# Optimization experiments

Measured on AMD Instinct MI355X. Metric: run time of the kernel, lower is better.

Reference implementation:

```python
import jax, jax.numpy as jnp
import numpy as np

B, T, ROLL, RHY, COND, Z1, H = 4096, 32, 130, 3, 12, 128, 1024
IN1 = Z1 + ROLL + RHY + COND  # 273, grucell_1 input size


def _gru_cell(x, h, w_ih, w_hh, b_ih, b_hh):
    # PyTorch GRUCell math. w_ih: [3H, in], w_hh: [3H, H]
    gi = x @ w_ih.T + b_ih
    gh = h @ w_hh.T + b_hh
    i_r, i_z, i_n = jnp.split(gi, 3, axis=1)
    h_r, h_z, h_n = jnp.split(gh, 3, axis=1)
    r = jax.nn.sigmoid(i_r + h_r)
    z = jax.nn.sigmoid(i_z + h_z)
    n = jnp.tanh(i_n + r * h_n)
    return (1.0 - z) * n + z * h


def setup_inputs() -> dict:
    key = jax.random.key(0)
    ks = jax.random.split(key, 20)
    s = 0.02
    inp = {
        "z1": jax.random.normal(ks[0], (B, Z1), jnp.float32),
        "dis1_mean": jax.random.normal(ks[1], (B, Z1), jnp.float32),
        "dis1_std": jax.random.uniform(ks[2], (B, Z1), jnp.float32),
        "dis2_mean": jax.random.normal(ks[3], (B, Z1), jnp.float32),
        "dis2_std": jax.random.uniform(ks[4], (B, Z1), jnp.float32),
        "recon_rhythm": jax.random.normal(ks[5], (B, T, RHY), jnp.float32),
        "sample": jax.random.normal(ks[6], (B, T, ROLL), jnp.float32),
        "condition": jax.random.normal(ks[7], (B, T, COND), jnp.float32),
        "iteration": 1000,
        # grucell_1
        "w_ih1": jax.random.normal(ks[8], (3 * H, IN1), jnp.float32) * s,
        "w_hh1": jax.random.normal(ks[9], (3 * H, H), jnp.float32) * s,
        "b_ih1": jax.random.normal(ks[10], (3 * H,), jnp.float32) * s,
        "b_hh1": jax.random.normal(ks[11], (3 * H,), jnp.float32) * s,
        # grucell_2
        "w_ih2": jax.random.normal(ks[12], (3 * H, H), jnp.float32) * s,
        "w_hh2": jax.random.normal(ks[13], (3 * H, H), jnp.float32) * s,
        "b_ih2": jax.random.normal(ks[14], (3 * H,), jnp.float32) * s,
        "b_hh2": jax.random.normal(ks[15], (3 * H,), jnp.float32) * s,
        # linear_init_1: z1 -> H
        "w_init": jax.random.normal(ks[16], (H, Z1), jnp.float32) * s,
        "b_init": jax.random.normal(ks[17], (H,), jnp.float32) * s,
        # linear_out_1: H -> roll
        "w_out": jax.random.normal(ks[18], (ROLL, H), jnp.float32) * s,
        "b_out": jax.random.normal(ks[19], (ROLL,), jnp.float32) * s,
    }
    return inp


def reference(z1, dis1_mean, dis1_std, dis2_mean, dis2_std, recon_rhythm, sample,
              condition, iteration, w_ih1, w_hh1, b_ih1, b_hh1, w_ih2, w_hh2,
              b_ih2, b_hh2, w_init, b_init, w_out, b_out):
    # Eval-mode final_decoder: teacher forcing off, argmax one-hot sampling.
    h1_0 = jnp.tanh(z1 @ w_init.T + b_init)
    out0 = jnp.zeros((B, ROLL), z1.dtype).at[:, -1].set(1.0)
    h2_0 = jnp.zeros((B, H), z1.dtype)  # overwritten at step 0

    rhy_t = jnp.transpose(recon_rhythm, (1, 0, 2))   # [T,B,RHY]
    cond_t = jnp.transpose(condition, (1, 0, 2))     # [T,B,COND]

    def step(carry, xs):
        out, h1, h2 = carry
        i, r_i, c_i = xs
        inp = jnp.concatenate([out, r_i, z1, c_i], axis=1)  # [B, IN1]
        h1 = _gru_cell(inp, h1, w_ih1, w_hh1, b_ih1, b_hh1)
        h2 = jnp.where(i == 0, h1, h2)  # hx[1] = hx[0] on first step
        h2 = _gru_cell(h1, h2, w_ih2, w_hh2, b_ih2, b_hh2)
        logp = jax.nn.log_softmax(h2 @ w_out.T + b_out, axis=1)  # [B,ROLL]
        out = jax.nn.one_hot(jnp.argmax(logp, axis=1), ROLL, dtype=logp.dtype)
        return (out, h1, h2), logp

    xs = (jnp.arange(T), rhy_t, cond_t)
    _, logps = jax.lax.scan(step, (out0, h1_0, h2_0), xs)
    recon = jnp.transpose(logps, (1, 0, 2))  # [B,T,ROLL]
    return (recon, recon_rhythm, dis1_mean, dis1_std, dis2_mean, dis2_std)
```

## Files before the change

### kernel.cpp

```cpp
#include <hip/hip_runtime.h>
#include <stdint.h>

typedef unsigned short u16;
typedef unsigned int u32;
typedef __attribute__((ext_vector_type(4))) float f32x4;
typedef __attribute__((ext_vector_type(8))) short short8;

#define MFMA16(a, b, c) __builtin_amdgcn_mfma_f32_16x16x32_bf16(a, b, c, 0, 0, 0)

#define B_SZ   4096
#define H_SZ   1024
#define T_SZ   32
#define NROLL  130
#define EXTK   192
#define NCPAD  144

__device__ __forceinline__ u16 f2b(float f) {
  u32 u = __float_as_uint(f);
  u += 0x7FFFu + ((u >> 16) & 1u);
  return (u16)(u >> 16);
}
__device__ __forceinline__ float sigm(float x) { return 1.f / (1.f + __expf(-x)); }

__device__ __forceinline__ void gld16(const void* g, const void* lds) {
  __builtin_amdgcn_global_load_lds(
      (const __attribute__((address_space(1))) u32*)(uintptr_t)g,
      (__attribute__((address_space(3))) u32*)(u32)(uintptr_t)lds, 16, 0, 0);
}

__global__ void cvt_kernel(const float* __restrict__ s, u16* __restrict__ d, int n) {
  int i = blockIdx.x * 256 + threadIdx.x;
  if (i < n) d[i] = f2b(s[i]);
}

__global__ void build_wout_kernel(const float* __restrict__ w, u16* __restrict__ d) {
  int i = blockIdx.x * 256 + threadIdx.x;
  int r = i >> 10, c = i & 1023;
  d[i] = f2b(r < NROLL ? w[r * H_SZ + c] : 0.f);
}

__global__ void build_wext_kernel(const float* __restrict__ w, u16* __restrict__ d) {
  int i = blockIdx.x * 256 + threadIdx.x;
  int j = i / EXTK, k = i % EXTK;
  float v = 0.f;
  if (k < 3)        v = w[j * 273 + 130 + k];
  else if (k < 15)  v = w[j * 273 + 261 + (k - 3)];
  else if (k < 143) v = w[j * 273 + 133 + (k - 15)];
  d[i] = f2b(v);
}

__global__ void build_wih1T_kernel(const float* __restrict__ w, float* __restrict__ d) {
  int i = blockIdx.x * 256 + threadIdx.x;
  if (i >= NROLL * 3072) return;
  int c = i / 3072, j = i % 3072;
  d[i] = w[j * 273 + c];
}

__global__ void build_aext_kernel(const float* __restrict__ rhy, const float* __restrict__ cond,
                                  const float* __restrict__ z1, u16* __restrict__ d) {
  long long i = (long long)blockIdx.x * 256 + threadIdx.x;
  int t = (int)(i / (B_SZ * EXTK));
  int r = (int)(i % (B_SZ * EXTK));
  int b = r / EXTK, k = r % EXTK;
  float v = 0.f;
  if (k < 3)        v = rhy[b * (T_SZ * 3) + t * 3 + k];
  else if (k < 15)  v = cond[b * (T_SZ * 12) + t * 12 + (k - 3)];
  else if (k < 143) v = z1[b * 128 + (k - 15)];
  d[i] = f2b(v);
}

__global__ void init_amax_kernel(int* __restrict__ a) {
  a[blockIdx.x * 256 + threadIdx.x] = NROLL - 1;
}

__global__ __launch_bounds__(256, 2)
void init_h1_mfma_kernel(const u16* __restrict__ Az,
                         const u16* __restrict__ Wz,
                         const float* __restrict__ b_init,
                         float* __restrict__ h1f, u16* __restrict__ h1b) {
  __shared__ u16 As[128 * 64];
  __shared__ u16 Ws[64 * 64];
  const int tid = threadIdx.x;
  const int lane = tid & 63, wv = tid >> 6;
  const int wm = wv >> 1, wn = wv & 1;
  const int lr = lane & 15, lk = lane >> 4;
  const int Mbase = blockIdx.x * 128, Nbase = blockIdx.y * 64;

  f32x4 zero = {0.f, 0.f, 0.f, 0.f};
  f32x4 acc[4][2];
#pragma unroll
  for (int m = 0; m < 4; ++m)
#pragma unroll
    for (int n = 0; n < 2; ++n) acc[m][n] = zero;

  for (int it = 0; it < 2; ++it) {
#pragma unroll
    for (int i = 0; i < 4; ++i) {
      int seg = i * 256 + tid, row = seg >> 3, c8 = seg & 7;
      gld16(Az + (size_t)(Mbase + row) * 128 + it * 64 + c8 * 8, As + ((i * 256 + (wv << 6)) << 3));
    }
#pragma unroll
    for (int i = 0; i < 2; ++i) {
      int seg = i * 256 + tid, row = seg >> 3, c8 = seg & 7;
      gld16(Wz + (size_t)(Nbase + row) * 128 + it * 64 + c8 * 8, Ws + ((i * 256 + (wv << 6)) << 3));
    }
    __syncthreads();
#pragma unroll
    for (int kk = 0; kk < 2; ++kk) {
      short8 af[4];
#pragma unroll
      for (int m = 0; m < 4; ++m)
        af[m] = *(const short8*)(As + (((wm << 6) + (m << 4) + lr) << 6) + kk * 32 + (lk << 3));
      short8 bw[2];
#pragma unroll
      for (int n = 0; n < 2; ++n)
        bw[n] = *(const short8*)(Ws + ((((wn << 5) + (n << 4) + lr)) << 6) + kk * 32 + (lk << 3));
#pragma unroll
      for (int m = 0; m < 4; ++m)
#pragma unroll
        for (int n = 0; n < 2; ++n)
          acc[m][n] = MFMA16(af[m], bw[n], acc[m][n]);
    }
    __syncthreads();
  }

  int hcol[2];
  hcol[0] = Nbase + (wn << 5) + lr;
  hcol[1] = hcol[0] + 16;
#pragma unroll
  for (int m = 0; m < 4; ++m) {
#pragma unroll
    for (int q = 0; q < 4; ++q) {
      int b = Mbase + (wm << 6) + (m << 4) + (lk << 2) + q;
      size_t ho = (size_t)b << 10;
#pragma unroll
      for (int n = 0; n < 2; ++n) {
        int h = hcol[n];
        float v = tanhf(acc[m][n][q] + b_init[h]);
        h1f[ho + h] = v;
        h1b[ho + h] = f2b(v);
      }
    }
  }
}

__global__ __launch_bounds__(256, 2)
void gru1_kernel(const u16* __restrict__ Ah,
                 const u16* __restrict__ Whh,
                 const u16* __restrict__ Ae,
                 const u16* __restrict__ Wex,
                 const float* __restrict__ gT,
                 const float* __restrict__ bih, const float* __restrict__ bhh,
                 const int* __restrict__ amax,
                 float* __restrict__ h1f, u16* __restrict__ h1o) {
  __shared__ u16 smem[40960];
  u16* As = smem;
  u16* Wsm = smem + 16384;
  const int tid = threadIdx.x;
  const int lane = tid & 63, wv = tid >> 6;
  const int wm = wv >> 1, wn = wv & 1;
  const int lr = lane & 15, lk = lane >> 4;
  const int Mbase = blockIdx.x * 128, Nbase = blockIdx.y * 64;

  f32x4 zero = {0.f, 0.f, 0.f, 0.f};
  f32x4 acc_r[4][2], acc_z[4][2], acc_hn[4][2], acc_in[4][2];
#pragma unroll
  for (int m = 0; m < 4; ++m)
#pragma unroll
    for (int n = 0; n < 2; ++n) { acc_r[m][n] = zero; acc_z[m][n] = zero; acc_hn[m][n] = zero; acc_in[m][n] = zero; }

#pragma unroll 1
  for (int it = 0; it < 8; ++it) {
#pragma unroll
    for (int i = 0; i < 8; ++i) {
      int seg = i * 256 + tid, row = seg >> 4, c16 = (seg & 15) ^ (row & 7);
      gld16(Ah + (size_t)(Mbase + row) * 1024 + it * 128 + c16 * 8, As + ((i * 256 + (wv << 6)) << 3));
    }
#pragma unroll
    for (int i = 0; i < 12; ++i) {
      int seg = i * 256 + tid, gr = seg >> 4, c16 = (seg & 15) ^ (gr & 7);
      int gg = gr >> 6, r = gr & 63;
      gld16(Whh + ((size_t)(gg << 10) + Nbase + r) * 1024 + it * 128 + c16 * 8,
            Wsm + ((i * 256 + (wv << 6)) << 3));
    }
    __syncthreads();
    __builtin_amdgcn_s_setprio(1);
#pragma unroll
    for (int kk = 0; kk < 4; ++kk) {
      int gc = (kk << 2) + lk;
      short8 af[4];
#pragma unroll
      for (int m = 0; m < 4; ++m) {
        int row = (wm << 6) + (m << 4) + lr;
        af[m] = *(const short8*)(As + (row << 7) + ((gc ^ (row & 7)) << 3));
      }
      short8 bw[3][2];
#pragma unroll
      for (int g = 0; g < 3; ++g)
#pragma unroll
        for (int n = 0; n < 2; ++n) {
          int row = (g << 6) + (wn << 5) + (n << 4) + lr;
          bw[g][n] = *(const short8*)(Wsm + (row << 7) + ((gc ^ (row & 7)) << 3));
        }
#pragma unroll
      for (int m = 0; m < 4; ++m)
#pragma unroll
        for (int n = 0; n < 2; ++n) {
          acc_r[m][n] = MFMA16(af[m], bw[0][n], acc_r[m][n]);
          acc_z[m][n] = MFMA16(af[m], bw[1][n], acc_z[m][n]);
          acc_hn[m][n] = MFMA16(af[m], bw[2][n], acc_hn[m][n]);
        }
    }
    __builtin_amdgcn_s_setprio(0);
    __syncthreads();
  }

#pragma unroll 1
  for (int e = 0; e < 3; ++e) {
#pragma unroll
    for (int i = 0; i < 4; ++i) {
      int seg = i * 256 + tid, row = seg >> 3, c8 = (seg & 7) ^ (row & 7);
      gld16(Ae + (size_t)(Mbase + row) * EXTK + e * 64 + c8 * 8, As + ((i * 256 + (wv << 6)) << 3));
    }
#pragma unroll
    for (int i = 0; i < 6; ++i) {
      int seg = i * 256 + tid, gr = seg >> 3, c8 = (seg & 7) ^ (gr & 7);
      int gg = gr >> 6, r = gr & 63;
      gld16(Wex + ((size_t)(gg << 10) + Nbase + r) * EXTK + e * 64 + c8 * 8,
            Wsm + ((i * 256 + (wv << 6)) << 3));
    }
    __syncthreads();
    __builtin_amdgcn_s_setprio(1);
#pragma unroll
    for (int kk = 0; kk < 2; ++kk) {
      int gc = (kk << 2) + lk;
      short8 af[4];
#pragma unroll
      for (int m = 0; m < 4; ++m) {
        int row = (wm << 6) + (m << 4) + lr;
        af[m] = *(const short8*)(As + (row << 6) + ((gc ^ (row & 7)) << 3));
      }
      short8 bw[3][2];
#pragma unroll
      for (int g = 0; g < 3; ++g)
#pragma unroll
        for (int n = 0; n < 2; ++n) {
          int row = (g << 6) + (wn << 5) + (n << 4) + lr;
          bw[g][n] = *(const short8*)(Wsm + (row << 6) + ((gc ^ (row & 7)) << 3));
        }
#pragma unroll
      for (int m = 0; m < 4; ++m)
#pragma unroll
        for (int n = 0; n < 2; ++n) {
          acc_r[m][n] = MFMA16(af[m], bw[0][n], acc_r[m][n]);
          acc_z[m][n] = MFMA16(af[m], bw[1][n], acc_z[m][n]);
          acc_in[m][n] = MFMA16(af[m], bw[2][n], acc_in[m][n]);
        }
    }
    __builtin_amdgcn_s_setprio(0);
    __syncthreads();
  }

  int hcol[2];
  hcol[0] = Nbase + (wn << 5) + lr;
  hcol[1] = hcol[0] + 16;
  float bi0[2], bi1[2], bi2[2], bh0[2], bh1[2], bh2[2];
#pragma unroll
  for (int n = 0; n < 2; ++n) {
    int h = hcol[n];
    bi0[n] = bih[h]; bi1[n] = bih[1024 + h]; bi2[n] = bih[2048 + h];
    bh0[n] = bhh[h]; bh1[n] = bhh[1024 + h]; bh2[n] = bhh[2048 + h];
  }
#pragma unroll
  for (int m = 0; m < 4; ++m) {
#pragma unroll
    for (int q = 0; q < 4; ++q) {
      int b = Mbase + (wm << 6) + (m << 4) + (lk << 2) + q;
      const float* gRow = gT + (size_t)amax[b] * 3072;
      size_t ho = (size_t)b << 10;
#pragma unroll
      for (int n = 0; n < 2; ++n) {
        int h = hcol[n];
        float rp = acc_r[m][n][q] + bi0[n] + bh0[n] + gRow[h];
        float zp = acc_z[m][n][q] + bi1[n] + bh1[n] + gRow[1024 + h];
        float inp = acc_in[m][n][q] + bi2[n] + gRow[2048 + h];
        float hnp = acc_hn[m][n][q] + bh2[n];
        float r = sigm(rp), z = sigm(zp);
        float nn = tanhf(inp + r * hnp);
        float hv = (1.f - z) * nn + z * h1f[ho + h];
        h1f[ho + h] = hv;
        h1o[ho + h] = f2b(hv);
      }
    }
  }
}

__global__ __launch_bounds__(256, 2)
void gru2_kernel(const u16* __restrict__ A1,
                 const u16* __restrict__ A2,
                 const u16* __restrict__ Wi,
                 const u16* __restrict__ Wh,
                 const float* __restrict__ bih, const float* __restrict__ bhh,
                 const float* __restrict__ hpf,
                 float* __restrict__ h2f, u16* __restrict__ h2o) {
  __shared__ u16 As1[128 * 64];
  __shared__ u16 As2[128 * 64];
  __shared__ u16 Ws[384 * 64];
  const int tid = threadIdx.x;
  const int lane = tid & 63, wv = tid >> 6;
  const int wm = wv >> 1, wn = wv & 1;
  const int lr = lane & 15, lk = lane >> 4;
  const int Mbase = blockIdx.x * 128, Nbase = blockIdx.y * 64;

  f32x4 zero = {0.f, 0.f, 0.f, 0.f};
  f32x4 acc_r[4][2], acc_z[4][2], acc_hn[4][2], acc_in[4][2];
#pragma unroll
  for (int m = 0; m < 4; ++m)
#pragma unroll
    for (int n = 0; n < 2; ++n) { acc_r[m][n] = zero; acc_z[m][n] = zero; acc_hn[m][n] = zero; acc_in[m][n] = zero; }

#pragma unroll 1
  for (int it = 0; it < 16; ++it) {
#pragma unroll
    for (int i = 0; i < 4; ++i) {
      int seg = i * 256 + tid, row = seg >> 3, c8 = (seg & 7) ^ (row & 7);
      size_t go = (size_t)(Mbase + row) * 1024 + it * 64 + c8 * 8;
      gld16(A1 + go, As1 + ((i * 256 + (wv << 6)) << 3));
      gld16(A2 + go, As2 + ((i * 256 + (wv << 6)) << 3));
    }
#pragma unroll
    for (int i = 0; i < 12; ++i) {
      int seg = i * 256 + tid, gr = seg >> 3, c8 = (seg & 7) ^ (gr & 7);
      int s = gr >> 6, r = gr & 63;
      const u16* Wm = (s < 3) ? Wi : Wh;
      int gate = (s < 3) ? s : (s - 3);
      gld16(Wm + ((size_t)(gate << 10) + Nbase + r) * 1024 + it * 64 + c8 * 8,
            Ws + ((i * 256 + (wv << 6)) << 3));
    }
    __syncthreads();
    __builtin_amdgcn_s_setprio(1);
#pragma unroll
    for (int kk = 0; kk < 2; ++kk) {
      int gc = (kk << 2) + lk;
      short8 a1[4], a2[4];
#pragma unroll
      for (int m = 0; m < 4; ++m) {
        int row = (wm << 6) + (m << 4) + lr;
        int off = (row << 6) + ((gc ^ (row & 7)) << 3);
        a1[m] = *(const short8*)(As1 + off);
        a2[m] = *(const short8*)(As2 + off);
      }
      short8 bw[6][2];
#pragma unroll
      for (int s = 0; s < 6; ++s)
#pragma unroll
        for (int n = 0; n < 2; ++n) {
          int row = (s << 6) + (wn << 5) + (n << 4) + lr;
          bw[s][n] = *(const short8*)(Ws + (row << 6) + ((gc ^ (row & 7)) << 3));
        }
#pragma unroll
      for (int m = 0; m < 4; ++m)
#pragma unroll
        for (int n = 0; n < 2; ++n) {
          acc_r[m][n] = MFMA16(a1[m], bw[0][n], acc_r[m][n]);
          acc_r[m][n] = MFMA16(a2[m], bw[3][n], acc_r[m][n]);
          acc_z[m][n] = MFMA16(a1[m], bw[1][n], acc_z[m][n]);
          acc_z[m][n] = MFMA16(a2[m], bw[4][n], acc_z[m][n]);
          acc_in[m][n] = MFMA16(a1[m], bw[2][n], acc_in[m][n]);
          acc_hn[m][n] = MFMA16(a2[m], bw[5][n], acc_hn[m][n]);
        }
    }
    __builtin_amdgcn_s_setprio(0);
    __syncthreads();
  }

  int hcol[2];
  hcol[0] = Nbase + (wn << 5) + lr;
  hcol[1] = hcol[0] + 16;
  float bi0[2], bi1[2], bi2[2], bh0[2], bh1[2], bh2[2];
#pragma unroll
  for (int n = 0; n < 2; ++n) {
    int h = hcol[n];
    bi0[n] = bih[h]; bi1[n] = bih[1024 + h]; bi2[n] = bih[2048 + h];
    bh0[n] = bhh[h]; bh1[n] = bhh[1024 + h]; bh2[n] = bhh[2048 + h];
  }
#pragma unroll
  for (int m = 0; m < 4; ++m) {
#pragma unroll
    for (int q = 0; q < 4; ++q) {
      int b = Mbase + (wm << 6) + (m << 4) + (lk << 2) + q;
      size_t ho = (size_t)b << 10;
#pragma unroll
      for (int n = 0; n < 2; ++n) {
        int h = hcol[n];
        float r = sigm(acc_r[m][n][q] + bi0[n] + bh0[n]);
        float z = sigm(acc_z[m][n][q] + bi1[n] + bh1[n]);
        float nn = tanhf(acc_in[m][n][q] + bi2[n] + r * (acc_hn[m][n][q] + bh2[n]));
        float hv = (1.f - z) * nn + z * hpf[ho + h];
        h2f[ho + h] = hv;
        h2o[ho + h] = f2b(hv);
      }
    }
  }
}

__global__ __launch_bounds__(128)
void out_kernel(const u16* __restrict__ A,
                const u16* __restrict__ W,
                const float* __restrict__ b_out,
                float* __restrict__ recon, int* __restrict__ amax_out, int t) {
  __shared__ u16 As[16 * 64];
  __shared__ u16 Ws[144 * 64];
  __shared__ float redm[2][16], reds[2][16], logZs[16];
  __shared__ int redi[2][16];
  const int tid = threadIdx.x;
  const int lane = tid & 63, wv = tid >> 6;
  const int lr = lane & 15, lk = lane >> 4;
  const int bb = blockIdx.x;
  const int nf0 = wv ? 5 : 0;
  const int nfn = wv ? 4 : 5;

  f32x4 zero = {0.f, 0.f, 0.f, 0.f};
  f32x4 acc[5];
#pragma unroll
  for (int j = 0; j < 5; ++j) acc[j] = zero;

  float bo[5];
#pragma unroll
  for (int j = 0; j < 5; ++j) {
    int col = ((nf0 + j) << 4) + lr;
    bo[j] = (j < nfn && col < NROLL) ? b_out[col] : -1e30f;
  }

#pragma unroll 1
  for (int it = 0; it < 16; ++it) {
    {
      int seg = tid, row = seg >> 3, c8 = seg & 7;
      gld16(A + (size_t)(bb * 16 + row) * 1024 + it * 64 + c8 * 8, As + ((wv << 6) << 3));
    }
#pragma unroll
    for (int i = 0; i < 9; ++i) {
      int seg = i * 128 + tid, row = seg >> 3, c8 = seg & 7;
      gld16(W + (size_t)row * 1024 + it * 64 + c8 * 8, Ws + ((i * 128 + (wv << 6)) << 3));
    }
    __syncthreads();
#pragma unroll
    for (int kk = 0; kk < 2; ++kk) {
      short8 af = *(const short8*)(As + (lr << 6) + kk * 32 + (lk << 3));
#pragma unroll 5
      for (int j = 0; j < 5; ++j) {
        if (j < nfn) {
          short8 bw = *(const short8*)(Ws + ((((nf0 + j) << 4) + lr) << 6) + kk * 32 + (lk << 3));
          acc[j] = MFMA16(af, bw, acc[j]);
        }
      }
    }
    __syncthreads();
  }

#pragma unroll
  for (int q = 0; q < 4; ++q) {
    int r = (lk << 2) + q;
    float vmax = -1e30f; int vidx = 0;
#pragma unroll 5
    for (int j = 0; j < 5; ++j) {
      if (j < nfn) {
        int col = ((nf0 + j) << 4) + lr;
        float x = acc[j][q] + bo[j];
        if (x > vmax) { vmax = x; vidx = col; }
      }
    }
    for (int d = 1; d < 16; d <<= 1) {
      float om = __shfl_xor(vmax, d);
      int oi = __shfl_xor(vidx, d);
      if (om > vmax || (om == vmax && oi < vidx)) { vmax = om; vidx = oi; }
    }
    float s = 0.f;
#pragma unroll 5
    for (int j = 0; j < 5; ++j) {
      if (j < nfn) s += __expf(acc[j][q] + bo[j] - vmax);
    }
    for (int d = 1; d < 16; d <<= 1) s += __shfl_xor(s, d);
    if (lr == 0) { redm[wv][r] = vmax; reds[wv][r] = s; redi[wv][r] = vidx; }
  }
  __syncthreads();

  if (tid < 16) {
    float m0 = redm[0][tid], m1 = redm[1][tid];
    float s0 = reds[0][tid], s1 = reds[1][tid];
    float M = fmaxf(m0, m1);
    float S = s0 * __expf(m0 - M) + s1 * __expf(m1 - M);
    logZs[tid] = M + __logf(S);
    amax_out[bb * 16 + tid] = (m1 > m0) ? redi[1][tid] : redi[0][tid];
  }
  __syncthreads();

#pragma unroll
  for (int q = 0; q < 4; ++q) {
    int r = (lk << 2) + q;
    int b = bb * 16 + r;
    float lz = logZs[r];
#pragma unroll 5
    for (int j = 0; j < 5; ++j) {
      if (j < nfn) {
        int col = ((nf0 + j) << 4) + lr;
        if (col < NROLL)
          recon[(size_t)b * (T_SZ * NROLL) + t * NROLL + col] = acc[j][q] + bo[j] - lz;
      }
    }
  }
}

extern "C" void kernel_launch(void* const* d_in, const int* in_sizes, int n_in,
                              void* d_out, int out_size, void* d_ws, size_t ws_size,
                              hipStream_t stream) {
  const float* z1    = (const float*)d_in[0];
  const float* d1m   = (const float*)d_in[1];
  const float* d1s   = (const float*)d_in[2];
  const float* d2m   = (const float*)d_in[3];
  const float* d2s   = (const float*)d_in[4];
  const float* rhy   = (const float*)d_in[5];
  const float* cond  = (const float*)d_in[7];
  const float* w_ih1 = (const float*)d_in[9];
  const float* w_hh1 = (const float*)d_in[10];
  const float* b_ih1 = (const float*)d_in[11];
  const float* b_hh1 = (const float*)d_in[12];
  const float* w_ih2 = (const float*)d_in[13];
  const float* w_hh2 = (const float*)d_in[14];
  const float* b_ih2 = (const float*)d_in[15];
  const float* b_hh2 = (const float*)d_in[16];
  const float* w_init = (const float*)d_in[17];
  const float* b_init = (const float*)d_in[18];
  const float* w_out  = (const float*)d_in[19];
  const float* b_out  = (const float*)d_in[20];
  float* out = (float*)d_out;

  char* ws = (char*)d_ws;
  size_t off = 0;
  auto alloc = [&](size_t bytes) -> void* {
    off = (off + 255) & ~(size_t)255;
    void* p = ws + off;
    off += bytes;
    return p;
  };
  u16* whh1_b = (u16*)alloc((size_t)3072 * 1024 * 2);
  u16* wih2_b = (u16*)alloc((size_t)3072 * 1024 * 2);
  u16* whh2_b = (u16*)alloc((size_t)3072 * 1024 * 2);
  u16* wout_b = (u16*)alloc((size_t)NCPAD * 1024 * 2);
  u16* wext_b = (u16*)alloc((size_t)3072 * EXTK * 2);
  float* wih1T = (float*)alloc((size_t)NROLL * 3072 * 4);
  u16* aext   = (u16*)alloc((size_t)T_SZ * B_SZ * EXTK * 2);
  float* h1f  = (float*)alloc((size_t)B_SZ * H_SZ * 4);
  float* h2f  = (float*)alloc((size_t)B_SZ * H_SZ * 4);
  u16* h1b[2];
  h1b[0] = (u16*)alloc((size_t)B_SZ * H_SZ * 2);
  h1b[1] = (u16*)alloc((size_t)B_SZ * H_SZ * 2);
  u16* h2b[2];
  h2b[0] = (u16*)alloc((size_t)B_SZ * H_SZ * 2);
  h2b[1] = (u16*)alloc((size_t)B_SZ * H_SZ * 2);
  int* amax = (int*)alloc((size_t)B_SZ * 4);
  u16* z1b    = (u16*)alloc((size_t)B_SZ * 128 * 2);
  u16* winitb = (u16*)alloc((size_t)H_SZ * 128 * 2);

  const int NW = 3072 * 1024;
  cvt_kernel<<<(NW + 255) / 256, 256, 0, stream>>>(w_hh1, whh1_b, NW);
  cvt_kernel<<<(NW + 255) / 256, 256, 0, stream>>>(w_ih2, wih2_b, NW);
  cvt_kernel<<<(NW + 255) / 256, 256, 0, stream>>>(w_hh2, whh2_b, NW);
  cvt_kernel<<<(B_SZ * 128 + 255) / 256, 256, 0, stream>>>(z1, z1b, B_SZ * 128);
  cvt_kernel<<<(H_SZ * 128 + 255) / 256, 256, 0, stream>>>(w_init, winitb, H_SZ * 128);
  build_wout_kernel<<<(NCPAD * 1024) / 256, 256, 0, stream>>>(w_out, wout_b);
  build_wext_kernel<<<(3072 * EXTK) / 256, 256, 0, stream>>>(w_ih1, wext_b);
  build_wih1T_kernel<<<(NROLL * 3072 + 255) / 256, 256, 0, stream>>>(w_ih1, wih1T);
  build_aext_kernel<<<(T_SZ * B_SZ * EXTK) / 256, 256, 0, stream>>>(rhy, cond, z1, aext);
  init_h1_mfma_kernel<<<dim3(B_SZ / 128, H_SZ / 64), 256, 0, stream>>>(z1b, winitb, b_init, h1f, h1b[0]);
  init_amax_kernel<<<B_SZ / 256, 256, 0, stream>>>(amax);

  size_t o_rhy = (size_t)B_SZ * T_SZ * NROLL;
  size_t o_d1m = o_rhy + (size_t)B_SZ * T_SZ * 3;
  size_t o_d1s = o_d1m + (size_t)B_SZ * 128;
  size_t o_d2m = o_d1s + (size_t)B_SZ * 128;
  size_t o_d2s = o_d2m + (size_t)B_SZ * 128;
  hipMemcpyAsync(out + o_rhy, rhy, (size_t)B_SZ * T_SZ * 3 * 4, hipMemcpyDeviceToDevice, stream);
  hipMemcpyAsync(out + o_d1m, d1m, (size_t)B_SZ * 128 * 4, hipMemcpyDeviceToDevice, stream);
  hipMemcpyAsync(out + o_d1s, d1s, (size_t)B_SZ * 128 * 4, hipMemcpyDeviceToDevice, stream);
  hipMemcpyAsync(out + o_d2m, d2m, (size_t)B_SZ * 128 * 4, hipMemcpyDeviceToDevice, stream);
  hipMemcpyAsync(out + o_d2s, d2s, (size_t)B_SZ * 128 * 4, hipMemcpyDeviceToDevice, stream);

  dim3 ggrid(B_SZ / 128, H_SZ / 64);
  for (int t = 0; t < T_SZ; ++t) {
    const u16* h1in = h1b[t & 1];
    u16* h1out = h1b[(t & 1) ^ 1];
    gru1_kernel<<<ggrid, 256, 0, stream>>>(h1in, whh1_b, aext + (size_t)t * B_SZ * EXTK,
                                           wext_b, wih1T, b_ih1, b_hh1, amax, h1f, h1out);
    const u16* h2in = (t == 0) ? (const u16*)h1out : h2b[t & 1];
    const float* hpf = (t == 0) ? h1f : h2f;
    u16* h2out = h2b[(t & 1) ^ 1];
    gru2_kernel<<<ggrid, 256, 0, stream>>>(h1out, h2in, wih2_b, whh2_b, b_ih2, b_hh2,
                                           hpf, h2f, h2out);
    out_kernel<<<B_SZ / 16, 128, 0, stream>>>(h2out, wout_b, b_out, out, amax, t);
  }
  (void)in_sizes; (void)n_in; (void)out_size; (void)ws_size;
}
```

Baseline: 3.663 ms.

## Prepack GRU2 weights in MFMA fragment order and load them directly from global

Adds a one-time prepass that packs w_ih2 and w_hh2 as bf16 in per-lane MFMA operand order. gru2_kernel then reads its B fragments straight from global memory with one coalesced 16-byte load per lane, and the LDS weight tile and its staging loads are removed. This cuts LDS traffic and shared-memory footprint, which may raise occupancy. The cost is weight loads issued inside the compute loop, no longer overlapped through LDS, and the two waves sharing an N-slice now fetch the same weights separately, relying on L2 to absorb it.

Result: slower. 4.462 ms (+21.8%).

```diff
diff --git a/kernel.cpp b/kernel.cpp
--- a/kernel.cpp
+++ b/kernel.cpp
@@ -67,6 +67,21 @@
   else if (k < 15)  v = cond[b * (T_SZ * 12) + t * 12 + (k - 3)];
   else if (k < 143) v = z1[b * 128 + (k - 15)];
   d[i] = f2b(v);
+}
+
+__global__ void build_wpk2_kernel(const float* __restrict__ wi, const float* __restrict__ wh,
+                                  u16* __restrict__ d) {
+  int i = blockIdx.x * 256 + threadIdx.x;
+  int j = i & 7;
+  int lane = (i >> 3) & 63;
+  int kb = (i >> 9) & 31;
+  int nb = (i >> 14) & 63;
+  int g = i >> 20;
+  int n = nb * 16 + (lane & 15);
+  int k = kb * 32 + (lane >> 4) * 8 + j;
+  const float* src = (g < 3) ? wi : wh;
+  int gg = (g < 3) ? g : g - 3;
+  d[i] = f2b(src[(size_t)(gg * 1024 + n) * 1024 + k]);
 }
 
 __global__ void init_amax_kernel(int* __restrict__ a) {
@@ -298,19 +313,18 @@
 __global__ __launch_bounds__(256, 2)
 void gru2_kernel(const u16* __restrict__ A1,
                  const u16* __restrict__ A2,
-                 const u16* __restrict__ Wi,
-                 const u16* __restrict__ Wh,
+                 const u16* __restrict__ Wpk,
                  const float* __restrict__ bih, const float* __restrict__ bhh,
                  const float* __restrict__ hpf,
                  float* __restrict__ h2f, u16* __restrict__ h2o) {
   __shared__ u16 As1[128 * 64];
   __shared__ u16 As2[128 * 64];
-  __shared__ u16 Ws[384 * 64];
   const int tid = threadIdx.x;
   const int lane = tid & 63, wv = tid >> 6;
   const int wm = wv >> 1, wn = wv & 1;
   const int lr = lane & 15, lk = lane >> 4;
   const int Mbase = blockIdx.x * 128, Nbase = blockIdx.y * 64;
+  const int nbB = (Nbase >> 4) + (wn << 1);
 
   f32x4 zero = {0.f, 0.f, 0.f, 0.f};
   f32x4 acc_r[4][2], acc_z[4][2], acc_hn[4][2], acc_in[4][2];
@@ -328,19 +342,17 @@
       gld16(A1 + go, As1 + ((i * 256 + (wv << 6)) << 3));
       gld16(A2 + go, As2 + ((i * 256 + (wv << 6)) << 3));
     }
-#pragma unroll
-    for (int i = 0; i < 12; ++i) {
-      int seg = i * 256 + tid, gr = seg >> 3, c8 = (seg & 7) ^ (gr & 7);
-      int s = gr >> 6, r = gr & 63;
-      const u16* Wm = (s < 3) ? Wi : Wh;
-      int gate = (s < 3) ? s : (s - 3);
-      gld16(Wm + ((size_t)(gate << 10) + Nbase + r) * 1024 + it * 64 + c8 * 8,
-            Ws + ((i * 256 + (wv << 6)) << 3));
-    }
     __syncthreads();
     __builtin_amdgcn_s_setprio(1);
 #pragma unroll
     for (int kk = 0; kk < 2; ++kk) {
+      int kb = (it << 1) + kk;
+      short8 bw[6][2];
+#pragma unroll
+      for (int g = 0; g < 6; ++g)
+#pragma unroll
+        for (int nf = 0; nf < 2; ++nf)
+          bw[g][nf] = *(const short8*)(Wpk + ((((size_t)((g << 6) + nbB + nf) << 5) + kb) << 9) + (lane << 3));
       int gc = (kk << 2) + lk;
       short8 a1[4], a2[4];
 #pragma unroll
@@ -350,14 +362,6 @@
         a1[m] = *(const short8*)(As1 + off);
         a2[m] = *(const short8*)(As2 + off);
       }
-      short8 bw[6][2];
-#pragma unroll
-      for (int s = 0; s < 6; ++s)
-#pragma unroll
-        for (int n = 0; n < 2; ++n) {
-          int row = (s << 6) + (wn << 5) + (n << 4) + lr;
-          bw[s][n] = *(const short8*)(Ws + (row << 6) + ((gc ^ (row & 7)) << 3));
-        }
 #pragma unroll
       for (int m = 0; m < 4; ++m)
 #pragma unroll
@@ -544,8 +548,7 @@
     return p;
   };
   u16* whh1_b = (u16*)alloc((size_t)3072 * 1024 * 2);
-  u16* wih2_b = (u16*)alloc((size_t)3072 * 1024 * 2);
-  u16* whh2_b = (u16*)alloc((size_t)3072 * 1024 * 2);
+  u16* wpk2   = (u16*)alloc((size_t)6 * 64 * 32 * 64 * 8 * 2);
   u16* wout_b = (u16*)alloc((size_t)NCPAD * 1024 * 2);
   u16* wext_b = (u16*)alloc((size_t)3072 * EXTK * 2);
   float* wih1T = (float*)alloc((size_t)NROLL * 3072 * 4);
@@ -564,8 +567,7 @@
 
   const int NW = 3072 * 1024;
   cvt_kernel<<<(NW + 255) / 256, 256, 0, stream>>>(w_hh1, whh1_b, NW);
-  cvt_kernel<<<(NW + 255) / 256, 256, 0, stream>>>(w_ih2, wih2_b, NW);
-  cvt_kernel<<<(NW + 255) / 256, 256, 0, stream>>>(w_hh2, whh2_b, NW);
+  build_wpk2_kernel<<<(6 * 64 * 32 * 64 * 8) / 256, 256, 0, stream>>>(w_ih2, w_hh2, wpk2);
   cvt_kernel<<<(B_SZ * 128 + 255) / 256, 256, 0, stream>>>(z1, z1b, B_SZ * 128);
   cvt_kernel<<<(H_SZ * 128 + 255) / 256, 256, 0, stream>>>(w_init, winitb, H_SZ * 128);
   build_wout_kernel<<<(NCPAD * 1024) / 256, 256, 0, stream>>>(w_out, wout_b);
@@ -595,7 +597,7 @@
     const u16* h2in = (t == 0) ? (const u16*)h1out : h2b[t & 1];
     const float* hpf = (t == 0) ? h1f : h2f;
     u16* h2out = h2b[(t & 1) ^ 1];
-    gru2_kernel<<<ggrid, 256, 0, stream>>>(h1out, h2in, wih2_b, whh2_b, b_ih2, b_hh2,
+    gru2_kernel<<<ggrid, 256, 0, stream>>>(h1out, h2in, wpk2, b_ih2, b_hh2,
                                            hpf, h2f, h2out);
     out_kernel<<<B_SZ / 16, 128, 0, stream>>>(h2out, wout_b, b_out, out, amax, t);
   }
```

## Shrink gru2 tile to 64 rows, split input/hidden passes; widen out_kernel K step

Applied to the files above, without the earlier changes.

The gru2 kernel now uses a 64-row M tile and processes the input and hidden weight GEMMs in two sequential passes, each staging only three gate slices. This cuts shared memory and accumulator registers, allows more resident blocks (launch bounds raised to 4) and doubles the grid size. The price is lower arithmetic intensity per loaded weight tile. The out_kernel now stages 128-wide K chunks, halving its loop iterations and barriers, at the cost of more shared memory per block.

Result: slower. 3.925 ms (+7.1%).

```diff
diff --git a/kernel.cpp b/kernel.cpp
--- a/kernel.cpp
+++ b/kernel.cpp
@@ -295,7 +295,7 @@
   }
 }
 
-__global__ __launch_bounds__(256, 2)
+__global__ __launch_bounds__(256, 4)
 void gru2_kernel(const u16* __restrict__ A1,
                  const u16* __restrict__ A2,
                  const u16* __restrict__ Wi,
@@ -303,75 +303,71 @@
                  const float* __restrict__ bih, const float* __restrict__ bhh,
                  const float* __restrict__ hpf,
                  float* __restrict__ h2f, u16* __restrict__ h2o) {
-  __shared__ u16 As1[128 * 64];
-  __shared__ u16 As2[128 * 64];
-  __shared__ u16 Ws[384 * 64];
+  __shared__ u16 As[64 * 64];
+  __shared__ u16 Ws[192 * 64];
   const int tid = threadIdx.x;
   const int lane = tid & 63, wv = tid >> 6;
   const int wm = wv >> 1, wn = wv & 1;
   const int lr = lane & 15, lk = lane >> 4;
-  const int Mbase = blockIdx.x * 128, Nbase = blockIdx.y * 64;
+  const int Mbase = blockIdx.x * 64, Nbase = blockIdx.y * 64;
 
   f32x4 zero = {0.f, 0.f, 0.f, 0.f};
-  f32x4 acc_r[4][2], acc_z[4][2], acc_hn[4][2], acc_in[4][2];
-#pragma unroll
-  for (int m = 0; m < 4; ++m)
-#pragma unroll
-    for (int n = 0; n < 2; ++n) { acc_r[m][n] = zero; acc_z[m][n] = zero; acc_hn[m][n] = zero; acc_in[m][n] = zero; }
-
+  f32x4 acc_r[2][2], acc_z[2][2], acc_in[2][2], acc_hn[2][2];
+#pragma unroll
+  for (int m = 0; m < 2; ++m)
+#pragma unroll
+    for (int n = 0; n < 2; ++n) { acc_r[m][n] = zero; acc_z[m][n] = zero; acc_in[m][n] = zero; acc_hn[m][n] = zero; }
+
+#pragma unroll
+  for (int p = 0; p < 2; ++p) {
+    const u16* Ap = p ? A2 : A1;
+    const u16* Wp = p ? Wh : Wi;
 #pragma unroll 1
-  for (int it = 0; it < 16; ++it) {
-#pragma unroll
-    for (int i = 0; i < 4; ++i) {
-      int seg = i * 256 + tid, row = seg >> 3, c8 = (seg & 7) ^ (row & 7);
-      size_t go = (size_t)(Mbase + row) * 1024 + it * 64 + c8 * 8;
-      gld16(A1 + go, As1 + ((i * 256 + (wv << 6)) << 3));
-      gld16(A2 + go, As2 + ((i * 256 + (wv << 6)) << 3));
-    }
-#pragma unroll
-    for (int i = 0; i < 12; ++i) {
-      int seg = i * 256 + tid, gr = seg >> 3, c8 = (seg & 7) ^ (gr & 7);
-      int s = gr >> 6, r = gr & 63;
-      const u16* Wm = (s < 3) ? Wi : Wh;
-      int gate = (s < 3) ? s : (s - 3);
-      gld16(Wm + ((size_t)(gate << 10) + Nbase + r) * 1024 + it * 64 + c8 * 8,
-            Ws + ((i * 256 + (wv << 6)) << 3));
-    }
-    __syncthreads();
-    __builtin_amdgcn_s_setprio(1);
-#pragma unroll
-    for (int kk = 0; kk < 2; ++kk) {
-      int gc = (kk << 2) + lk;
-      short8 a1[4], a2[4];
-#pragma unroll
-      for (int m = 0; m < 4; ++m) {
-        int row = (wm << 6) + (m << 4) + lr;
-        int off = (row << 6) + ((gc ^ (row & 7)) << 3);
-        a1[m] = *(const short8*)(As1 + off);
-        a2[m] = *(const short8*)(As2 + off);
-      }
-      short8 bw[6][2];
-#pragma unroll
-      for (int s = 0; s < 6; ++s)
-#pragma unroll
-        for (int n = 0; n < 2; ++n) {
-          int row = (s << 6) + (wn << 5) + (n << 4) + lr;
-          bw[s][n] = *(const short8*)(Ws + (row << 6) + ((gc ^ (row & 7)) << 3));
+    for (int it = 0; it < 16; ++it) {
+#pragma unroll
+      for (int i = 0; i < 2; ++i) {
+        int seg = i * 256 + tid, row = seg >> 3, c8 = (seg & 7) ^ (row & 7);
+        gld16(Ap + (size_t)(Mbase + row) * 1024 + it * 64 + c8 * 8, As + ((i * 256 + (wv << 6)) << 3));
+      }
+#pragma unroll
+      for (int i = 0; i < 6; ++i) {
+        int seg = i * 256 + tid, gr = seg >> 3, c8 = (seg & 7) ^ (gr & 7);
+        int g = gr >> 6, r = gr & 63;
+        gld16(Wp + ((size_t)((g << 10) + Nbase + r)) * 1024 + it * 64 + c8 * 8,
+              Ws + ((i * 256 + (wv << 6)) << 3));
+      }
+      __syncthreads();
+      __builtin_amdgcn_s_setprio(1);
+#pragma unroll
+      for (int kk = 0; kk < 2; ++kk) {
+        int gc = (kk << 2) + lk;
+        short8 af[2];
+#pragma unroll
+        for (int m = 0; m < 2; ++m) {
+          int row = (wm << 5) + (m << 4) + lr;
+          af[m] = *(const short8*)(As + (row << 6) + ((gc ^ (row & 7)) << 3));
         }
-#pragma unroll
-      for (int m = 0; m < 4; ++m)
-#pragma unroll
-        for (int n = 0; n < 2; ++n) {
-          acc_r[m][n] = MFMA16(a1[m], bw[0][n], acc_r[m][n]);
-          acc_r[m][n] = MFMA16(a2[m], bw[3][n], acc_r[m][n]);
-          acc_z[m][n] = MFMA16(a1[m], bw[1][n], acc_z[m][n]);
-          acc_z[m][n] = MFMA16(a2[m], bw[4][n], acc_z[m][n]);
-          acc_in[m][n] = MFMA16(a1[m], bw[2][n], acc_in[m][n]);
-          acc_hn[m][n] = MFMA16(a2[m], bw[5][n], acc_hn[m][n]);
-        }
-    }
-    __builtin_amdgcn_s_setprio(0);
-    __syncthreads();
+        short8 bw[3][2];
+#pragma unroll
+        for (int g = 0; g < 3; ++g)
+#pragma unroll
+          for (int n = 0; n < 2; ++n) {
+            int row = (g << 6) + (wn << 5) + (n << 4) + lr;
+            bw[g][n] = *(const short8*)(Ws + (row << 6) + ((gc ^ (row & 7)) << 3));
+          }
+#pragma unroll
+        for (int m = 0; m < 2; ++m)
+#pragma unroll
+          for (int n = 0; n < 2; ++n) {
+            acc_r[m][n] = MFMA16(af[m], bw[0][n], acc_r[m][n]);
+            acc_z[m][n] = MFMA16(af[m], bw[1][n], acc_z[m][n]);
+            if (p == 0) acc_in[m][n] = MFMA16(af[m], bw[2][n], acc_in[m][n]);
+            else        acc_hn[m][n] = MFMA16(af[m], bw[2][n], acc_hn[m][n]);
+          }
+      }
+      __builtin_amdgcn_s_setprio(0);
+      __syncthreads();
+    }
   }
 
   int hcol[2];
@@ -385,10 +381,10 @@
     bh0[n] = bhh[h]; bh1[n] = bhh[1024 + h]; bh2[n] = bhh[2048 + h];
   }
 #pragma unroll
-  for (int m = 0; m < 4; ++m) {
+  for (int m = 0; m < 2; ++m) {
 #pragma unroll
     for (int q = 0; q < 4; ++q) {
-      int b = Mbase + (wm << 6) + (m << 4) + (lk << 2) + q;
+      int b = Mbase + (wm << 5) + (m << 4) + (lk << 2) + q;
       size_t ho = (size_t)b << 10;
 #pragma unroll
       for (int n = 0; n < 2; ++n) {
@@ -409,8 +405,8 @@
                 const u16* __restrict__ W,
                 const float* __restrict__ b_out,
                 float* __restrict__ recon, int* __restrict__ amax_out, int t) {
-  __shared__ u16 As[16 * 64];
-  __shared__ u16 Ws[144 * 64];
+  __shared__ u16 As[16 * 128];
+  __shared__ u16 Ws[144 * 128];
   __shared__ float redm[2][16], reds[2][16], logZs[16];
   __shared__ int redi[2][16];
   const int tid = threadIdx.x;
@@ -433,24 +429,25 @@
   }
 
 #pragma unroll 1
-  for (int it = 0; it < 16; ++it) {
-    {
-      int seg = tid, row = seg >> 3, c8 = seg & 7;
-      gld16(A + (size_t)(bb * 16 + row) * 1024 + it * 64 + c8 * 8, As + ((wv << 6) << 3));
-    }
-#pragma unroll
-    for (int i = 0; i < 9; ++i) {
-      int seg = i * 128 + tid, row = seg >> 3, c8 = seg & 7;
-      gld16(W + (size_t)row * 1024 + it * 64 + c8 * 8, Ws + ((i * 128 + (wv << 6)) << 3));
-    }
-    __syncthreads();
-#pragma unroll
-    for (int kk = 0; kk < 2; ++kk) {
-      short8 af = *(const short8*)(As + (lr << 6) + kk * 32 + (lk << 3));
+  for (int it = 0; it < 8; ++it) {
+#pragma unroll
+    for (int i = 0; i < 2; ++i) {
+      int seg = i * 128 + tid, row = seg >> 4, c16 = seg & 15;
+      gld16(A + (size_t)(bb * 16 + row) * 1024 + it * 128 + c16 * 8, As + ((i * 128 + (wv << 6)) << 3));
+    }
+#pragma unroll
+    for (int i = 0; i < 18; ++i) {
+      int seg = i * 128 + tid, row = seg >> 4, c16 = seg & 15;
+      gld16(W + (size_t)row * 1024 + it * 128 + c16 * 8, Ws + ((i * 128 + (wv << 6)) << 3));
+    }
+    __syncthreads();
+#pragma unroll
+    for (int kk = 0; kk < 4; ++kk) {
+      short8 af = *(const short8*)(As + (lr << 7) + kk * 32 + (lk << 3));
 #pragma unroll 5
       for (int j = 0; j < 5; ++j) {
         if (j < nfn) {
-          short8 bw = *(const short8*)(Ws + ((((nf0 + j) << 4) + lr) << 6) + kk * 32 + (lk << 3));
+          short8 bw = *(const short8*)(Ws + ((((nf0 + j) << 4) + lr) << 7) + kk * 32 + (lk << 3));
           acc[j] = MFMA16(af, bw, acc[j]);
         }
       }
@@ -586,17 +583,18 @@
   hipMemcpyAsync(out + o_d2m, d2m, (size_t)B_SZ * 128 * 4, hipMemcpyDeviceToDevice, stream);
   hipMemcpyAsync(out + o_d2s, d2s, (size_t)B_SZ * 128 * 4, hipMemcpyDeviceToDevice, stream);
 
-  dim3 ggrid(B_SZ / 128, H_SZ / 64);
+  dim3 g1grid(B_SZ / 128, H_SZ / 64);
+  dim3 g2grid(B_SZ / 64, H_SZ / 64);
   for (int t = 0; t < T_SZ; ++t) {
     const u16* h1in = h1b[t & 1];
     u16* h1out = h1b[(t & 1) ^ 1];
-    gru1_kernel<<<ggrid, 256, 0, stream>>>(h1in, whh1_b, aext + (size_t)t * B_SZ * EXTK,
-                                           wext_b, wih1T, b_ih1, b_hh1, amax, h1f, h1out);
+    gru1_kernel<<<g1grid, 256, 0, stream>>>(h1in, whh1_b, aext + (size_t)t * B_SZ * EXTK,
+                                            wext_b, wih1T, b_ih1, b_hh1, amax, h1f, h1out);
     const u16* h2in = (t == 0) ? (const u16*)h1out : h2b[t & 1];
     const float* hpf = (t == 0) ? h1f : h2f;
     u16* h2out = h2b[(t & 1) ^ 1];
-    gru2_kernel<<<ggrid, 256, 0, stream>>>(h1out, h2in, wih2_b, whh2_b, b_ih2, b_hh2,
-                                           hpf, h2f, h2out);
+    gru2_kernel<<<g2grid, 256, 0, stream>>>(h1out, h2in, wih2_b, whh2_b, b_ih2, b_hh2,
+                                            hpf, h2f, h2out);
     out_kernel<<<B_SZ / 16, 128, 0, stream>>>(h2out, wout_b, b_out, out, amax, t);
   }
   (void)in_sizes; (void)n_in; (void)out_size; (void)ws_size;
```

## Precompute time-invariant z1 input projection once and widen out_kernel K tile

Applied to the files above, without the earlier changes.

The z1 part of the GRU1 input projection does not change across timesteps, so it is now computed once by a separate MFMA GEMM into a B x 3072 fp32 buffer. Each gru1 step then only does a small K=32 MFMA for rhythm and condition and adds the precomputed values in the epilogue. This removes about 128 of the 192 extended-K columns per step, at the cost of reading 4096x3072 floats per step. Separately, out_kernel now loads K tiles of 128 instead of 64, halving its loop iterations and barriers but using more LDS.

After: 3.632 ms. No clear change (-0.9%).

```diff
diff --git a/kernel.cpp b/kernel.cpp
--- a/kernel.cpp
+++ b/kernel.cpp
@@ -12,7 +12,6 @@
 #define H_SZ   1024
 #define T_SZ   32
 #define NROLL  130
-#define EXTK   192
 #define NCPAD  144
 
 __device__ __forceinline__ u16 f2b(float f) {
@@ -39,13 +38,30 @@
   d[i] = f2b(r < NROLL ? w[r * H_SZ + c] : 0.f);
 }
 
-__global__ void build_wext_kernel(const float* __restrict__ w, u16* __restrict__ d) {
+__global__ void build_wz1_kernel(const float* __restrict__ w, u16* __restrict__ d) {
   int i = blockIdx.x * 256 + threadIdx.x;
-  int j = i / EXTK, k = i % EXTK;
+  int j = i >> 7, k = i & 127;
+  d[i] = f2b(w[j * 273 + 133 + k]);
+}
+
+__global__ void build_wext15_kernel(const float* __restrict__ w, u16* __restrict__ d) {
+  int i = blockIdx.x * 256 + threadIdx.x;
+  int j = i >> 5, k = i & 31;
   float v = 0.f;
-  if (k < 3)        v = w[j * 273 + 130 + k];
-  else if (k < 15)  v = w[j * 273 + 261 + (k - 3)];
-  else if (k < 143) v = w[j * 273 + 133 + (k - 15)];
+  if (k < 3)       v = w[j * 273 + 130 + k];
+  else if (k < 15) v = w[j * 273 + 261 + (k - 3)];
+  d[i] = f2b(v);
+}
+
+__global__ void build_aext15_kernel(const float* __restrict__ rhy, const float* __restrict__ cond,
+                                    u16* __restrict__ d) {
+  int i = blockIdx.x * 256 + threadIdx.x;
+  int k = i & 31;
+  int b = (i >> 5) & 4095;
+  int t = i >> 17;
+  float v = 0.f;
+  if (k < 3)       v = rhy[b * (T_SZ * 3) + t * 3 + k];
+  else if (k < 15) v = cond[b * (T_SZ * 12) + t * 12 + (k - 3)];
   d[i] = f2b(v);
 }
 
@@ -56,21 +72,73 @@
   d[i] = w[j * 273 + c];
 }
 
-__global__ void build_aext_kernel(const float* __restrict__ rhy, const float* __restrict__ cond,
-                                  const float* __restrict__ z1, u16* __restrict__ d) {
-  long long i = (long long)blockIdx.x * 256 + threadIdx.x;
-  int t = (int)(i / (B_SZ * EXTK));
-  int r = (int)(i % (B_SZ * EXTK));
-  int b = r / EXTK, k = r % EXTK;
-  float v = 0.f;
-  if (k < 3)        v = rhy[b * (T_SZ * 3) + t * 3 + k];
-  else if (k < 15)  v = cond[b * (T_SZ * 12) + t * 12 + (k - 3)];
-  else if (k < 143) v = z1[b * 128 + (k - 15)];
-  d[i] = f2b(v);
-}
-
 __global__ void init_amax_kernel(int* __restrict__ a) {
   a[blockIdx.x * 256 + threadIdx.x] = NROLL - 1;
+}
+
+__global__ __launch_bounds__(256, 2)
+void bext_kernel(const u16* __restrict__ Az,
+                 const u16* __restrict__ Wz,
+                 float* __restrict__ bext) {
+  __shared__ u16 As[128 * 64];
+  __shared__ u16 Ws[64 * 64];
+  const int tid = threadIdx.x;
+  const int lane = tid & 63, wv = tid >> 6;
+  const int wm = wv >> 1, wn = wv & 1;
+  const int lr = lane & 15, lk = lane >> 4;
+  const int Mbase = blockIdx.x * 128, Nbase = blockIdx.y * 64;
+
+  f32x4 zero = {0.f, 0.f, 0.f, 0.f};
+  f32x4 acc[4][2];
+#pragma unroll
+  for (int m = 0; m < 4; ++m)
+#pragma unroll
+    for (int n = 0; n < 2; ++n) acc[m][n] = zero;
+
+  for (int it = 0; it < 2; ++it) {
+#pragma unroll
+    for (int i = 0; i < 4; ++i) {
+      int seg = i * 256 + tid, row = seg >> 3, c8 = seg & 7;
+      gld16(Az + (size_t)(Mbase + row) * 128 + it * 64 + c8 * 8, As + ((i * 256 + (wv << 6)) << 3));
+    }
+#pragma unroll
+    for (int i = 0; i < 2; ++i) {
+      int seg = i * 256 + tid, row = seg >> 3, c8 = seg & 7;
+      gld16(Wz + (size_t)(Nbase + row) * 128 + it * 64 + c8 * 8, Ws + ((i * 256 + (wv << 6)) << 3));
+    }
+    __syncthreads();
+#pragma unroll
+    for (int kk = 0; kk < 2; ++kk) {
+      short8 af[4];
+#pragma unroll
+      for (int m = 0; m < 4; ++m)
+        af[m] = *(const short8*)(As + (((wm << 6) + (m << 4) + lr) << 6) + kk * 32 + (lk << 3));
+      short8 bw[2];
+#pragma unroll
+      for (int n = 0; n < 2; ++n)
+        bw[n] = *(const short8*)(Ws + ((((wn << 5) + (n << 4) + lr)) << 6) + kk * 32 + (lk << 3));
+#pragma unroll
+      for (int m = 0; m < 4; ++m)
+#pragma unroll
+        for (int n = 0; n < 2; ++n)
+          acc[m][n] = MFMA16(af[m], bw[n], acc[m][n]);
+    }
+    __syncthreads();
+  }
+
+  int jcol[2];
+  jcol[0] = Nbase + (wn << 5) + lr;
+  jcol[1] = jcol[0] + 16;
+#pragma unroll
+  for (int m = 0; m < 4; ++m) {
+#pragma unroll
+    for (int q = 0; q < 4; ++q) {
+      int b = Mbase + (wm << 6) + (m << 4) + (lk << 2) + q;
+#pragma unroll
+      for (int n = 0; n < 2; ++n)
+        bext[(size_t)b * 3072 + jcol[n]] = acc[m][n][q];
+    }
+  }
 }
 
 __global__ __launch_bounds__(256, 2)
@@ -147,8 +215,9 @@
 __global__ __launch_bounds__(256, 2)
 void gru1_kernel(const u16* __restrict__ Ah,
                  const u16* __restrict__ Whh,
-                 const u16* __restrict__ Ae,
-                 const u16* __restrict__ Wex,
+                 const u16* __restrict__ A15,
+                 const u16* __restrict__ W15,
+                 const float* __restrict__ bext,
                  const float* __restrict__ gT,
                  const float* __restrict__ bih, const float* __restrict__ bhh,
                  const int* __restrict__ amax,
@@ -215,48 +284,43 @@
     __syncthreads();
   }
 
-#pragma unroll 1
-  for (int e = 0; e < 3; ++e) {
-#pragma unroll
-    for (int i = 0; i < 4; ++i) {
-      int seg = i * 256 + tid, row = seg >> 3, c8 = (seg & 7) ^ (row & 7);
-      gld16(Ae + (size_t)(Mbase + row) * EXTK + e * 64 + c8 * 8, As + ((i * 256 + (wv << 6)) << 3));
-    }
-#pragma unroll
-    for (int i = 0; i < 6; ++i) {
-      int seg = i * 256 + tid, gr = seg >> 3, c8 = (seg & 7) ^ (gr & 7);
+  {
+#pragma unroll
+    for (int i = 0; i < 2; ++i) {
+      int seg = i * 256 + tid, row = seg >> 2, c4 = (seg & 3) ^ (row & 3);
+      gld16(A15 + (size_t)(Mbase + row) * 32 + c4 * 8, As + ((i * 256 + (wv << 6)) << 3));
+    }
+#pragma unroll
+    for (int i = 0; i < 3; ++i) {
+      int seg = i * 256 + tid, gr = seg >> 2, c4 = (seg & 3) ^ (gr & 3);
       int gg = gr >> 6, r = gr & 63;
-      gld16(Wex + ((size_t)(gg << 10) + Nbase + r) * EXTK + e * 64 + c8 * 8,
+      gld16(W15 + ((size_t)(gg << 10) + Nbase + r) * 32 + c4 * 8,
             Wsm + ((i * 256 + (wv << 6)) << 3));
     }
     __syncthreads();
     __builtin_amdgcn_s_setprio(1);
-#pragma unroll
-    for (int kk = 0; kk < 2; ++kk) {
-      int gc = (kk << 2) + lk;
-      short8 af[4];
-#pragma unroll
-      for (int m = 0; m < 4; ++m) {
-        int row = (wm << 6) + (m << 4) + lr;
-        af[m] = *(const short8*)(As + (row << 6) + ((gc ^ (row & 7)) << 3));
-      }
-      short8 bw[3][2];
-#pragma unroll
-      for (int g = 0; g < 3; ++g)
-#pragma unroll
-        for (int n = 0; n < 2; ++n) {
-          int row = (g << 6) + (wn << 5) + (n << 4) + lr;
-          bw[g][n] = *(const short8*)(Wsm + (row << 6) + ((gc ^ (row & 7)) << 3));
-        }
-#pragma unroll
-      for (int m = 0; m < 4; ++m)
-#pragma unroll
-        for (int n = 0; n < 2; ++n) {
-          acc_r[m][n] = MFMA16(af[m], bw[0][n], acc_r[m][n]);
-          acc_z[m][n] = MFMA16(af[m], bw[1][n], acc_z[m][n]);
-          acc_in[m][n] = MFMA16(af[m], bw[2][n], acc_in[m][n]);
-        }
-    }
+    short8 af[4];
+#pragma unroll
+    for (int m = 0; m < 4; ++m) {
+      int row = (wm << 6) + (m << 4) + lr;
+      af[m] = *(const short8*)(As + (row << 5) + (((lk) ^ (row & 3)) << 3));
+    }
+    short8 bw[3][2];
+#pragma unroll
+    for (int g = 0; g < 3; ++g)
+#pragma unroll
+      for (int n = 0; n < 2; ++n) {
+        int row = (g << 6) + (wn << 5) + (n << 4) + lr;
+        bw[g][n] = *(const short8*)(Wsm + (row << 5) + (((lk) ^ (row & 3)) << 3));
+      }
+#pragma unroll
+    for (int m = 0; m < 4; ++m)
+#pragma unroll
+      for (int n = 0; n < 2; ++n) {
+        acc_r[m][n] = MFMA16(af[m], bw[0][n], acc_r[m][n]);
+        acc_z[m][n] = MFMA16(af[m], bw[1][n], acc_z[m][n]);
+        acc_in[m][n] = MFMA16(af[m], bw[2][n], acc_in[m][n]);
+      }
     __builtin_amdgcn_s_setprio(0);
     __syncthreads();
   }
@@ -277,13 +341,14 @@
     for (int q = 0; q < 4; ++q) {
       int b = Mbase + (wm << 6) + (m << 4) + (lk << 2) + q;
       const float* gRow = gT + (size_t)amax[b] * 3072;
+      const float* bx = bext + (size_t)b * 3072;
       size_t ho = (size_t)b << 10;
 #pragma unroll
       for (int n = 0; n < 2; ++n) {
         int h = hcol[n];
-        float rp = acc_r[m][n][q] + bi0[n] + bh0[n] + gRow[h];
-        float zp = acc_z[m][n][q] + bi1[n] + bh1[n] + gRow[1024 + h];
-        float inp = acc_in[m][n][q] + bi2[n] + gRow[2048 + h];
+        float rp = acc_r[m][n][q] + bi0[n] + bh0[n] + gRow[h] + bx[h];
+        float zp = acc_z[m][n][q] + bi1[n] + bh1[n] + gRow[1024 + h] + bx[1024 + h];
+        float inp = acc_in[m][n][q] + bi2[n] + gRow[2048 + h] + bx[2048 + h];
         float hnp = acc_hn[m][n][q] + bh2[n];
         float r = sigm(rp), z = sigm(zp);
         float nn = tanhf(inp + r * hnp);
@@ -409,8 +474,8 @@
                 const u16* __restrict__ W,
                 const float* __restrict__ b_out,
                 float* __restrict__ recon, int* __restrict__ amax_out, int t) {
-  __shared__ u16 As[16 * 64];
-  __shared__ u16 Ws[144 * 64];
+  __shared__ u16 As[16 * 128];
+  __shared__ u16 Ws[144 * 128];
   __shared__ float redm[2][16], reds[2][16], logZs[16];
   __shared__ int redi[2][16];
   const int tid = threadIdx.x;
@@ -433,24 +498,25 @@
   }
 
 #pragma unroll 1
-  for (int it = 0; it < 16; ++it) {
-    {
-      int seg = tid, row = seg >> 3, c8 = seg & 7;
-      gld16(A + (size_t)(bb * 16 + row) * 1024 + it * 64 + c8 * 8, As + ((wv << 6) << 3));
-    }
-#pragma unroll
-    for (int i = 0; i < 9; ++i) {
-      int seg = i * 128 + tid, row = seg >> 3, c8 = seg & 7;
-      gld16(W + (size_t)row * 1024 + it * 64 + c8 * 8, Ws + ((i * 128 + (wv << 6)) << 3));
-    }
-    __syncthreads();
-#pragma unroll
-    for (int kk = 0; kk < 2; ++kk) {
-      short8 af = *(const short8*)(As + (lr << 6) + kk * 32 + (lk << 3));
+  for (int it = 0; it < 8; ++it) {
+#pragma unroll
+    for (int i = 0; i < 2; ++i) {
+      int seg = i * 128 + tid, row = seg >> 4, c16 = seg & 15;
+      gld16(A + (size_t)(bb * 16 + row) * 1024 + it * 128 + c16 * 8, As + ((i * 128 + (wv << 6)) << 3));
+    }
+#pragma unroll
+    for (int i = 0; i < 18; ++i) {
+      int seg = i * 128 + tid, row = seg >> 4, c16 = seg & 15;
+      gld16(W + (size_t)row * 1024 + it * 128 + c16 * 8, Ws + ((i * 128 + (wv << 6)) << 3));
+    }
+    __syncthreads();
+#pragma unroll
+    for (int kk = 0; kk < 4; ++kk) {
+      short8 af = *(const short8*)(As + (lr << 7) + kk * 32 + (lk << 3));
 #pragma unroll 5
       for (int j = 0; j < 5; ++j) {
         if (j < nfn) {
-          short8 bw = *(const short8*)(Ws + ((((nf0 + j) << 4) + lr) << 6) + kk * 32 + (lk << 3));
+          short8 bw = *(const short8*)(Ws + ((((nf0 + j) << 4) + lr) << 7) + kk * 32 + (lk << 3));
           acc[j] = MFMA16(af, bw, acc[j]);
         }
       }
@@ -547,9 +613,11 @@
   u16* wih2_b = (u16*)alloc((size_t)3072 * 1024 * 2);
   u16* whh2_b = (u16*)alloc((size_t)3072 * 1024 * 2);
   u16* wout_b = (u16*)alloc((size_t)NCPAD * 1024 * 2);
-  u16* wext_b = (u16*)alloc((size_t)3072 * EXTK * 2);
+  u16* wz1_b  = (u16*)alloc((size_t)3072 * 128 * 2);
+  u16* w15_b  = (u16*)alloc((size_t)3072 * 32 * 2);
+  u16* a15    = (u16*)alloc((size_t)T_SZ * B_SZ * 32 * 2);
+  float* bext = (float*)alloc((size_t)B_SZ * 3072 * 4);
   float* wih1T = (float*)alloc((size_t)NROLL * 3072 * 4);
-  u16* aext   = (u16*)alloc((size_t)T_SZ * B_SZ * EXTK * 2);
   float* h1f  = (float*)alloc((size_t)B_SZ * H_SZ * 4);
   float* h2f  = (float*)alloc((size_t)B_SZ * H_SZ * 4);
   u16* h1b[2];
@@ -569,9 +637,11 @@
   cvt_kernel<<<(B_SZ * 128 + 255) / 256, 256, 0, stream>>>(z1, z1b, B_SZ * 128);
   cvt_kernel<<<(H_SZ * 128 + 255) / 256, 256, 0, stream>>>(w_init, winitb, H_SZ * 128);
   build_wout_kernel<<<(NCPAD * 1024) / 256, 256, 0, stream>>>(w_out, wout_b);
-  build_wext_kernel<<<(3072 * EXTK) / 256, 256, 0, stream>>>(w_ih1, wext_b);
+  build_wz1_kernel<<<(3072 * 128) / 256, 256, 0, stream>>>(w_ih1, wz1_b);
+  build_wext15_kernel<<<(3072 * 32) / 256, 256, 0, stream>>>(w_ih1, w15_b);
+  build_aext15_kernel<<<(T_SZ * B_SZ * 32) / 256, 256, 0, stream>>>(rhy, cond, a15);
   build_wih1T_kernel<<<(NROLL * 3072 + 255) / 256, 256, 0, stream>>>(w_ih1, wih1T);
-  build_aext_kernel<<<(T_SZ * B_SZ * EXTK) / 256, 256, 0, stream>>>(rhy, cond, z1, aext);
+  bext_kernel<<<dim3(B_SZ / 128, 3072 / 64), 256, 0, stream>>>(z1b, wz1_b, bext);
   init_h1_mfma_kernel<<<dim3(B_SZ / 128, H_SZ / 64), 256, 0, stream>>>(z1b, winitb, b_init, h1f, h1b[0]);
   init_amax_kernel<<<B_SZ / 256, 256, 0, stream>>>(amax);
 
@@ -590,8 +660,8 @@
   for (int t = 0; t < T_SZ; ++t) {
     const u16* h1in = h1b[t & 1];
     u16* h1out = h1b[(t & 1) ^ 1];
-    gru1_kernel<<<ggrid, 256, 0, stream>>>(h1in, whh1_b, aext + (size_t)t * B_SZ * EXTK,
-                                           wext_b, wih1T, b_ih1, b_hh1, amax, h1f, h1out);
+    gru1_kernel<<<ggrid, 256, 0, stream>>>(h1in, whh1_b, a15 + (size_t)t * B_SZ * 32,
+                                           w15_b, bext, wih1T, b_ih1, b_hh1, amax, h1f, h1out);
     const u16* h2in = (t == 0) ? (const u16*)h1out : h2b[t & 1];
     const float* hpf = (t == 0) ? h1f : h2f;
     u16* h2out = h2b[(t & 1) ^ 1];
```
